# Optimization experiments

Measured on AMD Instinct MI355X. Metric: run time of the kernel, lower is better.

Reference implementation:

```python
import jax, jax.numpy as jnp
import numpy as np

D_MODEL = 1024
NUM_HEADS = 16
HEAD_DIM = D_MODEL // NUM_HEADS


def setup_inputs() -> dict:
    key = jax.random.key(0)
    ks = jax.random.split(key, 5)
    B, S = 2, 2048
    x = jax.random.normal(ks[0], (B, S, D_MODEL), dtype=jnp.float32)
    Wq = jax.random.normal(ks[1], (D_MODEL, D_MODEL), dtype=jnp.float32) * 0.02
    Wk = jax.random.normal(ks[2], (D_MODEL, D_MODEL), dtype=jnp.float32) * 0.02
    Wv = jax.random.normal(ks[3], (D_MODEL, D_MODEL), dtype=jnp.float32) * 0.02
    Wo = jax.random.normal(ks[4], (D_MODEL, D_MODEL), dtype=jnp.float32) * 0.02
    return {"x": x, "Wq": Wq, "Wk": Wk, "Wv": Wv, "Wo": Wo}


def reference(x, Wq, Wk, Wv, Wo):
    B, S, _ = x.shape
    # QKV projections (Linear is x @ W, no bias)
    q = (x @ Wq).reshape(B, S, NUM_HEADS, HEAD_DIM).transpose(0, 2, 1, 3)  # [B,H,S,Dh]
    k = (x @ Wk).reshape(B, S, NUM_HEADS, HEAD_DIM).transpose(0, 2, 1, 3)
    v = (x @ Wv).reshape(B, S, NUM_HEADS, HEAD_DIM).transpose(0, 2, 1, 3)
    scale = 1.0 / jnp.sqrt(jnp.asarray(HEAD_DIM, dtype=x.dtype))
    scores = jnp.einsum("bhqd,bhkd->bhqk", q, k) * scale  # [B,H,S,S]
    causal = jnp.tril(jnp.ones((S, S), dtype=bool))
    scores = jnp.where(causal, scores, -jnp.inf)
    probs = jax.nn.softmax(scores, axis=-1)
    out = jnp.einsum("bhqk,bhkd->bhqd", probs, v)  # [B,H,S,Dh]
    out = out.transpose(0, 2, 1, 3).reshape(B, S, D_MODEL)
    return out @ Wo
```

## Files before the change

### kernel.cpp

```cpp
#include <hip/hip_runtime.h>

typedef __attribute__((ext_vector_type(4))) short short4v;
typedef __attribute__((ext_vector_type(8))) short short8v;
typedef __attribute__((ext_vector_type(4))) float float4v;
typedef __attribute__((ext_vector_type(4))) int int4v;

#define GLD_LDS16(gsrc, ldst)                                                             \
    __builtin_amdgcn_global_load_lds(                                                     \
        (const __attribute__((address_space(1))) void*)(gsrc),                            \
        (__attribute__((address_space(3))) void*)(ldst), 16, 0, 0)

__device__ __forceinline__ short f2bf(float f) {
    unsigned u = __builtin_bit_cast(unsigned, f);
    u += 0x7fffu + ((u >> 16) & 1u);
    return (short)(u >> 16);
}

__global__ void k_prep(const float* __restrict__ x, short* __restrict__ xb,
                       const float* __restrict__ W0, const float* __restrict__ W1,
                       const float* __restrict__ W2, const float* __restrict__ W3,
                       short* __restrict__ Wt) {
    __shared__ float tile[32][33];
    int bid = blockIdx.x;
    if (bid < 4096) {
        int i = bid * 256 + threadIdx.x;
        float4v v = ((const float4v*)x)[i];
        short4v o;
        o[0] = f2bf(v[0]); o[1] = f2bf(v[1]); o[2] = f2bf(v[2]); o[3] = f2bf(v[3]);
        ((short4v*)xb)[i] = o;
        return;
    }
    int L = bid - 4096;
    int z = L >> 10;
    int xy = L & 1023;
    int bx = xy & 31, by = xy >> 5;
    const float* W = z == 0 ? W0 : z == 1 ? W1 : z == 2 ? W2 : W3;
    short* dst = Wt + (size_t)z * 1024 * 1024;
    int x0 = bx * 32, y0 = by * 32;
    int tx = threadIdx.x & 31, ty = threadIdx.x >> 5;
#pragma unroll
    for (int j = 0; j < 4; j++) {
        int r = ty + j * 8;
        tile[r][tx] = W[(size_t)(y0 + r) * 1024 + x0 + tx];
    }
    __syncthreads();
#pragma unroll
    for (int j = 0; j < 4; j++) {
        int r = ty + j * 8;
        dst[(size_t)(x0 + r) * 1024 + y0 + tx] = f2bf(tile[tx][r]);
    }
}

__launch_bounds__(512, 4)
__global__ void k_gemmQKV(const short* __restrict__ A, const short* __restrict__ Wtb,
                          short* __restrict__ Qb, short* __restrict__ Kb,
                          short* __restrict__ Vtb) {
    __shared__ short As[2][128][64];
    __shared__ short Bs[2][128][64];
    int t = threadIdx.x;
    int l = t & 63, w = t >> 6;
    int wm = w >> 2, wn = w & 3;
    int lr = l & 15, lg = l >> 4;
    int m0 = blockIdx.x * 128;
    int nfull = blockIdx.y * 128;
    int which = nfull >> 10;
    int nb = nfull & 1023;

    int srow = l >> 3;
    int sg = (l & 7) ^ srow;
    const short* Ab0 = A + (size_t)(m0 + w * 8 + srow) * 1024 + sg * 8;
    const short* Ab1 = Ab0 + 64 * 1024;
    const short* Bb0 = Wtb + (size_t)(nfull + w * 8 + srow) * 1024 + sg * 8;
    const short* Bb1 = Bb0 + 64 * 1024;

    float4v acc[4][2] = {};

#define STAGE(bb, k0)                                   \
    do {                                                \
        GLD_LDS16(Ab0 + (k0), &As[bb][w * 8][0]);       \
        GLD_LDS16(Ab1 + (k0), &As[bb][64 + w * 8][0]);  \
        GLD_LDS16(Bb0 + (k0), &Bs[bb][w * 8][0]);       \
        GLD_LDS16(Bb1 + (k0), &Bs[bb][64 + w * 8][0]);  \
    } while (0)

    STAGE(0, 0);
    __syncthreads();
    int cur = 0;

    if (which == 2) {
        for (int kt = 0; kt < 16; kt++) {
            if (kt + 1 < 16) STAGE(cur ^ 1, (kt + 1) * 64);
#pragma unroll
            for (int ks = 0; ks < 2; ks++) {
                short8v af[4], bfv[2];
                int hh = ks * 4 + lg;
                int sw = ((hh ^ (lr & 7)) * 8);
#pragma unroll
                for (int fm = 0; fm < 4; fm++)
                    af[fm] = *(const short8v*)&As[cur][wm * 64 + fm * 16 + lr][sw];
#pragma unroll
                for (int fn = 0; fn < 2; fn++)
                    bfv[fn] = *(const short8v*)&Bs[cur][wn * 32 + fn * 16 + lr][sw];
                __builtin_amdgcn_s_setprio(1);
#pragma unroll
                for (int fm = 0; fm < 4; fm++)
#pragma unroll
                    for (int fn = 0; fn < 2; fn++)
                        acc[fm][fn] = __builtin_amdgcn_mfma_f32_16x16x32_bf16(bfv[fn], af[fm], acc[fm][fn], 0, 0, 0);
                __builtin_amdgcn_s_setprio(0);
            }
            __syncthreads();
            cur ^= 1;
        }
    } else {
        for (int kt = 0; kt < 16; kt++) {
            if (kt + 1 < 16) STAGE(cur ^ 1, (kt + 1) * 64);
#pragma unroll
            for (int ks = 0; ks < 2; ks++) {
                short8v af[4], bfv[2];
                int hh = ks * 4 + lg;
                int sw = ((hh ^ (lr & 7)) * 8);
#pragma unroll
                for (int fm = 0; fm < 4; fm++)
                    af[fm] = *(const short8v*)&As[cur][wm * 64 + fm * 16 + lr][sw];
#pragma unroll
                for (int fn = 0; fn < 2; fn++)
                    bfv[fn] = *(const short8v*)&Bs[cur][wn * 32 + fn * 16 + lr][sw];
                __builtin_amdgcn_s_setprio(1);
#pragma unroll
                for (int fm = 0; fm < 4; fm++)
#pragma unroll
                    for (int fn = 0; fn < 2; fn++)
                        acc[fm][fn] = __builtin_amdgcn_mfma_f32_16x16x32_bf16(af[fm], bfv[fn], acc[fm][fn], 0, 0, 0);
                __builtin_amdgcn_s_setprio(0);
            }
            __syncthreads();
            cur ^= 1;
        }
    }
#undef STAGE

    if (which < 2) {
        short* out = (which == 0) ? Qb : Kb;
        float scale = (which == 0) ? 0.125f * 1.44269504088896f : 1.0f;
#pragma unroll
        for (int fm = 0; fm < 4; fm++)
#pragma unroll
            for (int fn = 0; fn < 2; fn++)
#pragma unroll
                for (int r = 0; r < 4; r++) {
                    int m = m0 + wm * 64 + fm * 16 + lg * 4 + r;
                    int n = nb + wn * 32 + fn * 16 + lr;
                    float v = acc[fm][fn][r] * scale;
                    int b = m >> 11, s = m & 2047, h = n >> 6, dh = n & 63;
                    out[(((size_t)(b * 16 + h)) * 2048 + s) * 64 + dh] = f2bf(v);
                }
    } else {
#pragma unroll
        for (int fm = 0; fm < 4; fm++)
#pragma unroll
            for (int fn = 0; fn < 2; fn++)
#pragma unroll
                for (int r = 0; r < 4; r++) {
                    int n = nb + wn * 32 + fn * 16 + lg * 4 + r;
                    int m = m0 + wm * 64 + fm * 16 + lr;
                    int b = m >> 11, s = m & 2047, h = n >> 6, dh = n & 63;
                    Vtb[(((size_t)(b * 16 + h)) * 64 + dh) * 2048 + s] = f2bf(acc[fm][fn][r]);
                }
    }
}

__launch_bounds__(512, 4)
__global__ void k_gemmO(const short* __restrict__ A, const short* __restrict__ Bt,
                        float* __restrict__ outF) {
    __shared__ short As[2][128][64];
    __shared__ short Bs[2][128][64];
    int t = threadIdx.x;
    int l = t & 63, w = t >> 6;
    int wm = w >> 2, wn = w & 3;
    int lr = l & 15, lg = l >> 4;
    int m0 = blockIdx.x * 128, n0 = blockIdx.y * 128;

    int srow = l >> 3;
    int sg = (l & 7) ^ srow;
    const short* Ab0 = A + (size_t)(m0 + w * 8 + srow) * 1024 + sg * 8;
    const short* Ab1 = Ab0 + 64 * 1024;
    const short* Bb0 = Bt + (size_t)(n0 + w * 8 + srow) * 1024 + sg * 8;
    const short* Bb1 = Bb0 + 64 * 1024;

    float4v acc[4][2] = {};

#define STAGE(bb, k0)                                   \
    do {                                                \
        GLD_LDS16(Ab0 + (k0), &As[bb][w * 8][0]);       \
        GLD_LDS16(Ab1 + (k0), &As[bb][64 + w * 8][0]);  \
        GLD_LDS16(Bb0 + (k0), &Bs[bb][w * 8][0]);       \
        GLD_LDS16(Bb1 + (k0), &Bs[bb][64 + w * 8][0]);  \
    } while (0)

    STAGE(0, 0);
    __syncthreads();
    int cur = 0;

    for (int kt = 0; kt < 16; kt++) {
        if (kt + 1 < 16) STAGE(cur ^ 1, (kt + 1) * 64);
#pragma unroll
        for (int ks = 0; ks < 2; ks++) {
            short8v af[4], bfv[2];
            int hh = ks * 4 + lg;
            int sw = ((hh ^ (lr & 7)) * 8);
#pragma unroll
            for (int fm = 0; fm < 4; fm++)
                af[fm] = *(const short8v*)&As[cur][wm * 64 + fm * 16 + lr][sw];
#pragma unroll
            for (int fn = 0; fn < 2; fn++)
                bfv[fn] = *(const short8v*)&Bs[cur][wn * 32 + fn * 16 + lr][sw];
            __builtin_amdgcn_s_setprio(1);
#pragma unroll
            for (int fm = 0; fm < 4; fm++)
#pragma unroll
                for (int fn = 0; fn < 2; fn++)
                    acc[fm][fn] = __builtin_amdgcn_mfma_f32_16x16x32_bf16(af[fm], bfv[fn], acc[fm][fn], 0, 0, 0);
            __builtin_amdgcn_s_setprio(0);
        }
        __syncthreads();
        cur ^= 1;
    }
#undef STAGE

#pragma unroll
    for (int fm = 0; fm < 4; fm++)
#pragma unroll
        for (int fn = 0; fn < 2; fn++)
#pragma unroll
            for (int r = 0; r < 4; r++) {
                int m = m0 + wm * 64 + fm * 16 + lg * 4 + r;
                int n = n0 + wn * 32 + fn * 16 + lr;
                outF[(size_t)m * 1024 + n] = acc[fm][fn][r];
            }
}

__launch_bounds__(256, 2)
__global__ void k_attn(const short* __restrict__ Qb, const short* __restrict__ Kb,
                       const short* __restrict__ Vtb, short* __restrict__ Ob) {
    __shared__ short K_lds[2][64][64];
    __shared__ short V_lds[2][64][64];
    int t = threadIdx.x;
    int l = t & 63, w = t >> 6;
    int lr = l & 15, lg = l >> 4;

    int L = blockIdx.x;
    int bh = L & 31;
    int g = L >> 5;
    int p = (g < 8) ? g : 23 - g;
    int nch = 32 - p;

    const short* Qp = Qb + (size_t)bh * 2048 * 64;
    const short* Kp = Kb + (size_t)bh * 2048 * 64;
    const short* Vp = Vtb + (size_t)bh * 64 * 2048;

    auto stage = [&](int bb, int kv0) {
#pragma unroll
        for (int i = 0; i < 2; i++) {
            int s = t + i * 256;
            int row = s >> 3, cg = s & 7;
            int cs = (cg ^ (row & 7)) * 8;
            GLD_LDS16(&Kp[(size_t)(kv0 + row) * 64 + cs], (short*)K_lds[bb] + (size_t)s * 8);
            GLD_LDS16(&Vp[(size_t)row * 2048 + kv0 + cs], (short*)V_lds[bb] + (size_t)s * 8);
        }
    };

    stage(0, 0);

    int q0a = (31 - p) * 64 + w * 16;
    int q0b = p * 64 + w * 16;
    short8v qf0a = *(const short8v*)&Qp[(size_t)(q0a + lr) * 64 + lg * 8];
    short8v qf1a = *(const short8v*)&Qp[(size_t)(q0a + lr) * 64 + 32 + lg * 8];
    short8v qf0b = *(const short8v*)&Qp[(size_t)(q0b + lr) * 64 + lg * 8];
    short8v qf1b = *(const short8v*)&Qp[(size_t)(q0b + lr) * 64 + 32 + lg * 8];

    float4v oa[4] = {}, ob[4] = {};
    float mra = -3e38f, mrb = -3e38f;
    float lsa = 0.f, lsb = 0.f;
    int cur = 0;
    int b = bh >> 4, h = bh & 15;
    int g0 = lg >> 1;
    int hb = (lg & 1) * 4;

    auto softmax_pack = [&](float4v (&s)[4], float& mr, float& ls, float4v (&o)[4],
                            short8v& pa0, short8v& pa1) {
        float mx = -3e38f;
#pragma unroll
        for (int t4 = 0; t4 < 4; t4++)
#pragma unroll
            for (int r = 0; r < 4; r++) mx = fmaxf(mx, s[t4][r]);

        if (!__all(mx - mr <= 8.f)) {
            float m_ = fmaxf(mx, __shfl_xor(mx, 16));
            m_ = fmaxf(m_, __shfl_xor(m_, 32));
            float mnew = fmaxf(mr, m_);
            float sc = __builtin_amdgcn_exp2f(mr - mnew);
            mr = mnew;
            ls *= sc;
#pragma unroll
            for (int r = 0; r < 4; r++) {
                float scq = __shfl(sc, lg * 4 + r);
                o[0][r] *= scq; o[1][r] *= scq; o[2][r] *= scq; o[3][r] *= scq;
            }
        }
        unsigned d[8];
#pragma unroll
        for (int t4 = 0; t4 < 4; t4++) {
            float e0 = __builtin_amdgcn_exp2f(s[t4][0] - mr);
            float e1 = __builtin_amdgcn_exp2f(s[t4][1] - mr);
            float e2 = __builtin_amdgcn_exp2f(s[t4][2] - mr);
            float e3 = __builtin_amdgcn_exp2f(s[t4][3] - mr);
            ls += (e0 + e1) + (e2 + e3);
            asm("v_cvt_pk_bf16_f32 %0, %1, %2" : "=v"(d[2 * t4])     : "v"(e0), "v"(e1));
            asm("v_cvt_pk_bf16_f32 %0, %1, %2" : "=v"(d[2 * t4 + 1]) : "v"(e2), "v"(e3));
        }
        pa0 = __builtin_bit_cast(short8v, int4v{(int)d[0], (int)d[1], (int)d[2], (int)d[3]});
        pa1 = __builtin_bit_cast(short8v, int4v{(int)d[4], (int)d[5], (int)d[6], (int)d[7]});
    };

    __syncthreads();

    for (int ci = 0; ci < nch; ci++) {
        int kv0 = ci * 64;
        bool dual = (ci <= p);

        if (ci + 1 < nch) stage(cur ^ 1, (ci + 1) * 64);

        const short* Kf = (const short*)K_lds[cur];
        float4v sa[4] = {}, sb[4] = {};
        __builtin_amdgcn_s_setprio(1);
#pragma unroll
        for (int t4 = 0; t4 < 4; t4++) {
            int krow = t4 * 16 + lr;
            int sw = (krow & 7);
            short8v kfa = *(const short8v*)&Kf[krow * 64 + ((lg ^ sw) * 8)];
            short8v kfb = *(const short8v*)&Kf[krow * 64 + (((lg ^ 4) ^ sw) * 8)];
            sa[t4] = __builtin_amdgcn_mfma_f32_16x16x32_bf16(kfa, qf0a, sa[t4], 0, 0, 0);
            sa[t4] = __builtin_amdgcn_mfma_f32_16x16x32_bf16(kfb, qf1a, sa[t4], 0, 0, 0);
            if (dual) {
                sb[t4] = __builtin_amdgcn_mfma_f32_16x16x32_bf16(kfa, qf0b, sb[t4], 0, 0, 0);
                sb[t4] = __builtin_amdgcn_mfma_f32_16x16x32_bf16(kfb, qf1b, sb[t4], 0, 0, 0);
            }
        }
        __builtin_amdgcn_s_setprio(0);

        if (kv0 + 63 > q0a) {
#pragma unroll
            for (int t4 = 0; t4 < 4; t4++)
#pragma unroll
                for (int r = 0; r < 4; r++)
                    if (kv0 + t4 * 16 + 4 * lg + r > q0a + lr) sa[t4][r] = -3e38f;
        }
        if (dual && kv0 + 63 > q0b) {
#pragma unroll
            for (int t4 = 0; t4 < 4; t4++)
#pragma unroll
                for (int r = 0; r < 4; r++)
                    if (kv0 + t4 * 16 + 4 * lg + r > q0b + lr) sb[t4][r] = -3e38f;
        }

        short8v pa0, pa1, pb0, pb1;
        softmax_pack(sa, mra, lsa, oa, pa0, pa1);
        if (dual) softmax_pack(sb, mrb, lsb, ob, pb0, pb1);

        const short* Vf = (const short*)V_lds[cur];
        __builtin_amdgcn_s_setprio(1);
#pragma unroll
        for (int dt = 0; dt < 4; dt++) {
            int vrow = dt * 16 + lr;
            int sw = (vrow & 7);
            const short* Vr = Vf + vrow * 64;
            short4v a0 = *(const short4v*)&Vr[((g0    ) ^ sw) * 8 + hb];
            short4v a1 = *(const short4v*)&Vr[((g0 + 2) ^ sw) * 8 + hb];
            short4v b0 = *(const short4v*)&Vr[((g0 + 4) ^ sw) * 8 + hb];
            short4v b1 = *(const short4v*)&Vr[((g0 + 6) ^ sw) * 8 + hb];
            short8v vfa, vfb;
            vfa[0] = a0[0]; vfa[1] = a0[1]; vfa[2] = a0[2]; vfa[3] = a0[3];
            vfa[4] = a1[0]; vfa[5] = a1[1]; vfa[6] = a1[2]; vfa[7] = a1[3];
            vfb[0] = b0[0]; vfb[1] = b0[1]; vfb[2] = b0[2]; vfb[3] = b0[3];
            vfb[4] = b1[0]; vfb[5] = b1[1]; vfb[6] = b1[2]; vfb[7] = b1[3];
            oa[dt] = __builtin_amdgcn_mfma_f32_16x16x32_bf16(pa0, vfa, oa[dt], 0, 0, 0);
            oa[dt] = __builtin_amdgcn_mfma_f32_16x16x32_bf16(pa1, vfb, oa[dt], 0, 0, 0);
            if (dual) {
                ob[dt] = __builtin_amdgcn_mfma_f32_16x16x32_bf16(pb0, vfa, ob[dt], 0, 0, 0);
                ob[dt] = __builtin_amdgcn_mfma_f32_16x16x32_bf16(pb1, vfb, ob[dt], 0, 0, 0);
            }
        }
        __builtin_amdgcn_s_setprio(0);

        __syncthreads();
        cur ^= 1;
    }

    float la = lsa, lb = lsb;
    la += __shfl_xor(la, 16); la += __shfl_xor(la, 32);
    lb += __shfl_xor(lb, 16); lb += __shfl_xor(lb, 32);
    float inva_ = 1.0f / la, invb_ = 1.0f / lb;
    float inva[4], invb[4];
#pragma unroll
    for (int r = 0; r < 4; r++) {
        inva[r] = __shfl(inva_, lg * 4 + r);
        invb[r] = __shfl(invb_, lg * 4 + r);
    }
#pragma unroll
    for (int dt = 0; dt < 4; dt++)
#pragma unroll
        for (int r = 0; r < 4; r++) {
            int qa = q0a + lg * 4 + r;
            int qb = q0b + lg * 4 + r;
            Ob[((size_t)(b * 2048 + qa)) * 1024 + h * 64 + dt * 16 + lr] = f2bf(oa[dt][r] * inva[r]);
            Ob[((size_t)(b * 2048 + qb)) * 1024 + h * 64 + dt * 16 + lr] = f2bf(ob[dt][r] * invb[r]);
        }
}

extern "C" void kernel_launch(void* const* d_in, const int* in_sizes, int n_in,
                              void* d_out, int out_size, void* d_ws, size_t ws_size,
                              hipStream_t stream) {
    const float* x  = (const float*)d_in[0];
    const float* Wq = (const float*)d_in[1];
    const float* Wk = (const float*)d_in[2];
    const float* Wv = (const float*)d_in[3];
    const float* Wo = (const float*)d_in[4];
    float* out = (float*)d_out;

    char* ws = (char*)d_ws;
    short* xb  = (short*)(ws);
    short* Wtb = (short*)(ws + 8388608);
    short* Qb  = (short*)(ws + 16777216);
    short* Kb  = (short*)(ws + 25165824);
    short* Vtb = (short*)(ws + 33554432);
    short* Ob  = (short*)(ws + 41943040);

    k_prep<<<8192, 256, 0, stream>>>(x, xb, Wq, Wk, Wv, Wo, Wtb);
    k_gemmQKV<<<dim3(32, 24), 512, 0, stream>>>(xb, Wtb, Qb, Kb, Vtb);
    k_attn<<<512, 256, 0, stream>>>(Qb, Kb, Vtb, Ob);
    k_gemmO<<<dim3(32, 8), 512, 0, stream>>>(Ob, Wtb + 3 * 1048576, out);
}
```

Measured before the change: 105.2 us.

## Use 4 waves per block with 64x64 warp tiles in projection GEMMs

Both projection GEMMs drop from 8 waves (64x32 per wave) to 4 waves (64x64 per wave) per 128x128 block. Each wave now holds a 4x4 accumulator grid, so every LDS fragment load feeds more MFMAs, and the global-to-LDS staging is redistributed across 256 threads. The QKV kernel's duplicated k-loops are merged into one loop that branches on the output type inside. The cost is fewer waves to hide latency and more registers per thread.

```diff
diff --git a/kernel.cpp b/kernel.cpp
--- a/kernel.cpp
+++ b/kernel.cpp
@@ -51,7 +51,7 @@
     }
 }
 
-__launch_bounds__(512, 4)
+__launch_bounds__(256, 2)
 __global__ void k_gemmQKV(const short* __restrict__ A, const short* __restrict__ Wtb,
                           short* __restrict__ Qb, short* __restrict__ Kb,
                           short* __restrict__ Vtb) {
@@ -59,84 +59,75 @@
     __shared__ short Bs[2][128][64];
     int t = threadIdx.x;
     int l = t & 63, w = t >> 6;
-    int wm = w >> 2, wn = w & 3;
+    int wm = w >> 1, wn = w & 1;
     int lr = l & 15, lg = l >> 4;
     int m0 = blockIdx.x * 128;
     int nfull = blockIdx.y * 128;
     int which = nfull >> 10;
     int nb = nfull & 1023;
 
-    int srow = l >> 3;
-    int sg = (l & 7) ^ srow;
-    const short* Ab0 = A + (size_t)(m0 + w * 8 + srow) * 1024 + sg * 8;
-    const short* Ab1 = Ab0 + 64 * 1024;
-    const short* Bb0 = Wtb + (size_t)(nfull + w * 8 + srow) * 1024 + sg * 8;
-    const short* Bb1 = Bb0 + 64 * 1024;
-
-    float4v acc[4][2] = {};
-
-#define STAGE(bb, k0)                                   \
-    do {                                                \
-        GLD_LDS16(Ab0 + (k0), &As[bb][w * 8][0]);       \
-        GLD_LDS16(Ab1 + (k0), &As[bb][64 + w * 8][0]);  \
-        GLD_LDS16(Bb0 + (k0), &Bs[bb][w * 8][0]);       \
-        GLD_LDS16(Bb1 + (k0), &Bs[bb][64 + w * 8][0]);  \
+    int srow = t >> 3;
+    int cs = (((t & 7) ^ (srow & 7)) * 8);
+    const short* Ag[4];
+    const short* Bg[4];
+    int ldof[4];
+#pragma unroll
+    for (int i = 0; i < 4; i++) {
+        int row = srow + i * 32;
+        Ag[i] = A + (size_t)(m0 + row) * 1024 + cs;
+        Bg[i] = Wtb + (size_t)(nfull + row) * 1024 + cs;
+        ldof[i] = (t + i * 256) * 8;
+    }
+
+    float4v acc[4][4] = {};
+
+#define STAGE(bb, k0)                                                         \
+    do {                                                                      \
+        _Pragma("unroll")                                                     \
+        for (int i = 0; i < 4; i++) {                                         \
+            GLD_LDS16(Ag[i] + (k0), (short*)As[bb] + ldof[i]);                \
+            GLD_LDS16(Bg[i] + (k0), (short*)Bs[bb] + ldof[i]);                \
+        }                                                                     \
     } while (0)
 
     STAGE(0, 0);
     __syncthreads();
     int cur = 0;
 
-    if (which == 2) {
-        for (int kt = 0; kt < 16; kt++) {
-            if (kt + 1 < 16) STAGE(cur ^ 1, (kt + 1) * 64);
-#pragma unroll
-            for (int ks = 0; ks < 2; ks++) {
-                short8v af[4], bfv[2];
-                int hh = ks * 4 + lg;
-                int sw = ((hh ^ (lr & 7)) * 8);
+    for (int kt = 0; kt < 16; kt++) {
+        if (kt + 1 < 16) STAGE(cur ^ 1, (kt + 1) * 64);
+#pragma unroll
+        for (int ks = 0; ks < 2; ks++) {
+            short8v af[4], bfv[4];
+            int hh = ks * 4 + lg;
+#pragma unroll
+            for (int fm = 0; fm < 4; fm++) {
+                int ra = wm * 64 + fm * 16 + lr;
+                af[fm] = *(const short8v*)&As[cur][ra][((hh ^ (ra & 7)) * 8)];
+            }
+#pragma unroll
+            for (int fn = 0; fn < 4; fn++) {
+                int rb = wn * 64 + fn * 16 + lr;
+                bfv[fn] = *(const short8v*)&Bs[cur][rb][((hh ^ (rb & 7)) * 8)];
+            }
+            __builtin_amdgcn_s_setprio(1);
+            if (which == 2) {
 #pragma unroll
                 for (int fm = 0; fm < 4; fm++)
-                    af[fm] = *(const short8v*)&As[cur][wm * 64 + fm * 16 + lr][sw];
-#pragma unroll
-                for (int fn = 0; fn < 2; fn++)
-                    bfv[fn] = *(const short8v*)&Bs[cur][wn * 32 + fn * 16 + lr][sw];
-                __builtin_amdgcn_s_setprio(1);
+#pragma unroll
+                    for (int fn = 0; fn < 4; fn++)
+                        acc[fm][fn] = __builtin_amdgcn_mfma_f32_16x16x32_bf16(bfv[fn], af[fm], acc[fm][fn], 0, 0, 0);
+            } else {
 #pragma unroll
                 for (int fm = 0; fm < 4; fm++)
 #pragma unroll
-                    for (int fn = 0; fn < 2; fn++)
-                        acc[fm][fn] = __builtin_amdgcn_mfma_f32_16x16x32_bf16(bfv[fn], af[fm], acc[fm][fn], 0, 0, 0);
-                __builtin_amdgcn_s_setprio(0);
-            }
-            __syncthreads();
-            cur ^= 1;
-        }
-    } else {
-        for (int kt = 0; kt < 16; kt++) {
-            if (kt + 1 < 16) STAGE(cur ^ 1, (kt + 1) * 64);
-#pragma unroll
-            for (int ks = 0; ks < 2; ks++) {
-                short8v af[4], bfv[2];
-                int hh = ks * 4 + lg;
-                int sw = ((hh ^ (lr & 7)) * 8);
-#pragma unroll
-                for (int fm = 0; fm < 4; fm++)
-                    af[fm] = *(const short8v*)&As[cur][wm * 64 + fm * 16 + lr][sw];
-#pragma unroll
-                for (int fn = 0; fn < 2; fn++)
-                    bfv[fn] = *(const short8v*)&Bs[cur][wn * 32 + fn * 16 + lr][sw];
-                __builtin_amdgcn_s_setprio(1);
-#pragma unroll
-                for (int fm = 0; fm < 4; fm++)
-#pragma unroll
-                    for (int fn = 0; fn < 2; fn++)
+                    for (int fn = 0; fn < 4; fn++)
                         acc[fm][fn] = __builtin_amdgcn_mfma_f32_16x16x32_bf16(af[fm], bfv[fn], acc[fm][fn], 0, 0, 0);
-                __builtin_amdgcn_s_setprio(0);
-            }
-            __syncthreads();
-            cur ^= 1;
-        }
+            }
+            __builtin_amdgcn_s_setprio(0);
+        }
+        __syncthreads();
+        cur ^= 1;
     }
 #undef STAGE
 
@@ -146,11 +137,11 @@
 #pragma unroll
         for (int fm = 0; fm < 4; fm++)
 #pragma unroll
-            for (int fn = 0; fn < 2; fn++)
+            for (int fn = 0; fn < 4; fn++)
 #pragma unroll
                 for (int r = 0; r < 4; r++) {
                     int m = m0 + wm * 64 + fm * 16 + lg * 4 + r;
-                    int n = nb + wn * 32 + fn * 16 + lr;
+                    int n = nb + wn * 64 + fn * 16 + lr;
                     float v = acc[fm][fn][r] * scale;
                     int b = m >> 11, s = m & 2047, h = n >> 6, dh = n & 63;
                     out[(((size_t)(b * 16 + h)) * 2048 + s) * 64 + dh] = f2bf(v);
@@ -159,10 +150,10 @@
 #pragma unroll
         for (int fm = 0; fm < 4; fm++)
 #pragma unroll
-            for (int fn = 0; fn < 2; fn++)
+            for (int fn = 0; fn < 4; fn++)
 #pragma unroll
                 for (int r = 0; r < 4; r++) {
-                    int n = nb + wn * 32 + fn * 16 + lg * 4 + r;
+                    int n = nb + wn * 64 + fn * 16 + lg * 4 + r;
                     int m = m0 + wm * 64 + fm * 16 + lr;
                     int b = m >> 11, s = m & 2047, h = n >> 6, dh = n & 63;
                     Vtb[(((size_t)(b * 16 + h)) * 64 + dh) * 2048 + s] = f2bf(acc[fm][fn][r]);
@@ -170,32 +161,39 @@
     }
 }
 
-__launch_bounds__(512, 4)
+__launch_bounds__(256, 2)
 __global__ void k_gemmO(const short* __restrict__ A, const short* __restrict__ Bt,
                         float* __restrict__ outF) {
     __shared__ short As[2][128][64];
     __shared__ short Bs[2][128][64];
     int t = threadIdx.x;
     int l = t & 63, w = t >> 6;
-    int wm = w >> 2, wn = w & 3;
+    int wm = w >> 1, wn = w & 1;
     int lr = l & 15, lg = l >> 4;
     int m0 = blockIdx.x * 128, n0 = blockIdx.y * 128;
 
-    int srow = l >> 3;
-    int sg = (l & 7) ^ srow;
-    const short* Ab0 = A + (size_t)(m0 + w * 8 + srow) * 1024 + sg * 8;
-    const short* Ab1 = Ab0 + 64 * 1024;
-    const short* Bb0 = Bt + (size_t)(n0 + w * 8 + srow) * 1024 + sg * 8;
-    const short* Bb1 = Bb0 + 64 * 1024;
-
-    float4v acc[4][2] = {};
-
-#define STAGE(bb, k0)                                   \
-    do {                                                \
-        GLD_LDS16(Ab0 + (k0), &As[bb][w * 8][0]);       \
-        GLD_LDS16(Ab1 + (k0), &As[bb][64 + w * 8][0]);  \
-        GLD_LDS16(Bb0 + (k0), &Bs[bb][w * 8][0]);       \
-        GLD_LDS16(Bb1 + (k0), &Bs[bb][64 + w * 8][0]);  \
+    int srow = t >> 3;
+    int cs = (((t & 7) ^ (srow & 7)) * 8);
+    const short* Ag[4];
+    const short* Bg[4];
+    int ldof[4];
+#pragma unroll
+    for (int i = 0; i < 4; i++) {
+        int row = srow + i * 32;
+        Ag[i] = A + (size_t)(m0 + row) * 1024 + cs;
+        Bg[i] = Bt + (size_t)(n0 + row) * 1024 + cs;
+        ldof[i] = (t + i * 256) * 8;
+    }
+
+    float4v acc[4][4] = {};
+
+#define STAGE(bb, k0)                                                         \
+    do {                                                                      \
+        _Pragma("unroll")                                                     \
+        for (int i = 0; i < 4; i++) {                                         \
+            GLD_LDS16(Ag[i] + (k0), (short*)As[bb] + ldof[i]);                \
+            GLD_LDS16(Bg[i] + (k0), (short*)Bs[bb] + ldof[i]);                \
+        }                                                                     \
     } while (0)
 
     STAGE(0, 0);
@@ -206,20 +204,23 @@
         if (kt + 1 < 16) STAGE(cur ^ 1, (kt + 1) * 64);
 #pragma unroll
         for (int ks = 0; ks < 2; ks++) {
-            short8v af[4], bfv[2];
+            short8v af[4], bfv[4];
             int hh = ks * 4 + lg;
-            int sw = ((hh ^ (lr & 7)) * 8);
+#pragma unroll
+            for (int fm = 0; fm < 4; fm++) {
+                int ra = wm * 64 + fm * 16 + lr;
+                af[fm] = *(const short8v*)&As[cur][ra][((hh ^ (ra & 7)) * 8)];
+            }
+#pragma unroll
+            for (int fn = 0; fn < 4; fn++) {
+                int rb = wn * 64 + fn * 16 + lr;
+                bfv[fn] = *(const short8v*)&Bs[cur][rb][((hh ^ (rb & 7)) * 8)];
+            }
+            __builtin_amdgcn_s_setprio(1);
 #pragma unroll
             for (int fm = 0; fm < 4; fm++)
-                af[fm] = *(const short8v*)&As[cur][wm * 64 + fm * 16 + lr][sw];
-#pragma unroll
-            for (int fn = 0; fn < 2; fn++)
-                bfv[fn] = *(const short8v*)&Bs[cur][wn * 32 + fn * 16 + lr][sw];
-            __builtin_amdgcn_s_setprio(1);
-#pragma unroll
-            for (int fm = 0; fm < 4; fm++)
-#pragma unroll
-                for (int fn = 0; fn < 2; fn++)
+#pragma unroll
+                for (int fn = 0; fn < 4; fn++)
                     acc[fm][fn] = __builtin_amdgcn_mfma_f32_16x16x32_bf16(af[fm], bfv[fn], acc[fm][fn], 0, 0, 0);
             __builtin_amdgcn_s_setprio(0);
         }
@@ -231,11 +232,11 @@
 #pragma unroll
     for (int fm = 0; fm < 4; fm++)
 #pragma unroll
-        for (int fn = 0; fn < 2; fn++)
+        for (int fn = 0; fn < 4; fn++)
 #pragma unroll
             for (int r = 0; r < 4; r++) {
                 int m = m0 + wm * 64 + fm * 16 + lg * 4 + r;
-                int n = n0 + wn * 32 + fn * 16 + lr;
+                int n = n0 + wn * 64 + fn * 16 + lr;
                 outF[(size_t)m * 1024 + n] = acc[fm][fn][r];
             }
 }
@@ -437,7 +438,7 @@
     short* Ob  = (short*)(ws + 41943040);
 
     k_prep<<<8192, 256, 0, stream>>>(x, xb, Wq, Wk, Wv, Wo, Wtb);
-    k_gemmQKV<<<dim3(32, 24), 512, 0, stream>>>(xb, Wtb, Qb, Kb, Vtb);
+    k_gemmQKV<<<dim3(32, 24), 256, 0, stream>>>(xb, Wtb, Qb, Kb, Vtb);
     k_attn<<<512, 256, 0, stream>>>(Qb, Kb, Vtb, Ob);
-    k_gemmO<<<dim3(32, 8), 512, 0, stream>>>(Ob, Wtb + 3 * 1048576, out);
-}
+    k_gemmO<<<dim3(32, 8), 256, 0, stream>>>(Ob, Wtb + 3 * 1048576, out);
+}
```

Measured after the change: 112.4 us. 6.8% more time.
